# Optimization experiments

Hardware: AMD Instinct MI355X
Metric: run time of the kernel (lower is better)

The kernel has to match this reference:

```python
import jax, jax.numpy as jnp
import numpy as np

L_OBS = 512                      # number_of_obs
FOV = 6.283185307179586          # full 360-degree scan
EPS_PAR = 1e-4                   # parallel-ray threshold (matches torch |rxs|<0.0001)
MAP_SIZE = 256.0
B = 8
N = 8192


def setup_inputs() -> dict:
    key = jax.random.key(0)
    k1, k2, k3 = jax.random.split(key, 3)
    # map line segments: (x3, y3, x4, y4) in [0, 256]^2
    line_seg = jax.random.uniform(k1, (N, 4), dtype=jnp.float32) * MAP_SIZE
    # poses: xy in the map interior, theta in [0, 2pi)
    xy = MAP_SIZE * 0.25 + jax.random.uniform(k2, (B, 2), dtype=jnp.float32) * (MAP_SIZE * 0.5)
    theta = jax.random.uniform(k3, (B, 1), dtype=jnp.float32) * (2.0 * np.pi)
    pose = jnp.concatenate([xy, theta], axis=-1)
    return {"line_seg": line_seg, "pose": pose}


def _sense(line_seg, pose):
    # rays(): beam angles for each pose -> [B, L]
    beam = jnp.arange(L_OBS, dtype=jnp.float32) * (FOV / L_OBS)        # [L]
    ang = beam[None, :] + pose[:, 2:3]                                  # [B, L]
    rx = jnp.cos(ang)[:, :, None]                                       # [B, L, 1]
    ry = jnp.sin(ang)[:, :, None]
    x1 = pose[:, 0][:, None, None]                                      # [B, 1, 1]
    y1 = pose[:, 1][:, None, None]

    x3 = line_seg[:, 0][None, None, :]                                  # [1, 1, N]
    y3 = line_seg[:, 1][None, None, :]
    x4 = line_seg[:, 2][None, None, :]
    y4 = line_seg[:, 3][None, None, :]
    sx = x4 - x3
    sy = y4 - y3
    x1_x3 = x1 - x3                                                     # [B, 1, N]
    y1_y3 = y1 - y3

    # ray/segment intersection parameters, broadcast to [B, L, N]
    num_a = sx * y1_y3 - sy * x1_x3
    num_b = rx * y1_y3 - ry * x1_x3
    rxs = sy * rx - sx * ry
    parallel = jnp.abs(rxs) < EPS_PAR
    safe_rxs = jnp.where(parallel, jnp.float32(1.0), rxs)
    u_a = jnp.where(parallel, jnp.float32(0.0), num_a / safe_rxs)       # [B, L, N]
    u_b = jnp.where(parallel, jnp.float32(0.0), num_b / safe_rxs)

    valid = (~parallel) & (u_b >= 0.0) & (u_b <= 1.0) & (u_a >= 0.0)
    # nearest valid hit along each ray (torch: +1e7 penalty then nanargmin)
    u_masked = jnp.where(valid, u_a, jnp.float32(jnp.inf))
    idx = jnp.argmin(u_masked, axis=-1)                                 # [B, L]
    u_sel = jnp.take_along_axis(u_a, idx[:, :, None], axis=-1)          # [B, L, 1]

    ix = x1[:, :, 0] + rx[:, :, 0] * u_sel[:, :, 0]                     # [B, L]
    iy = y1[:, :, 0] + ry[:, :, 0] * u_sel[:, :, 0]
    return jnp.stack([ix, iy], axis=-1)                                 # [B, L, 2]


def _to_sensor_frame(pose, obs_global):
    c0 = pose[:, None, 0:2]                                             # [B, 1, 2]
    cos = jnp.cos(pose[:, 2])
    sin = jnp.sin(pose[:, 2])
    # R = [[cos, -sin], [sin, cos]] per batch, obs_local = (obs - c0) @ R
    R = jnp.stack([jnp.stack([cos, -sin], -1), jnp.stack([sin, cos], -1)], -2)  # [B, 2, 2]
    return jnp.einsum('blj,bjk->blk', obs_global - c0, R)


def reference(line_seg, pose):
    obs_global = _sense(line_seg, pose)
    obs_local = _to_sensor_frame(pose, obs_global)
    return obs_global, obs_local
```

## Files before the change

kernel.cpp:

```cpp
#include <hip/hip_runtime.h>
#include <math.h>

#define L_OBS   512
#define NSEG    8192
#define NB      8
#define EPS_PAR 1e-4f
#define ANG_STEP 0.012271846644580566f

#define SC2   32
#define CSEG2 (NSEG / SC2)
#define PART2_FLOATS (SC2 * NB * L_OBS)

__global__ __launch_bounds__(512) void raycast8_kernel(
    const float4* __restrict__ seg, const float* __restrict__ pose,
    float* __restrict__ part) {
    __shared__ float4 s4[CSEG2];
    __shared__ float  s_red[8][128];

    const int gid = blockIdx.x;
    const int sc = gid & (SC2 - 1);
    const int bg = (gid >> 5) & 3;
    const int b  = gid >> 7;

    const float x1 = pose[b * 3 + 0];
    const float y1 = pose[b * 3 + 1];
    const float th = pose[b * 3 + 2];

    const int t = threadIdx.x;
    if (t < CSEG2) {
        float4 v = seg[sc * CSEG2 + t];
        s4[t] = make_float4(v.z - v.x, v.w - v.y, x1 - v.x, y1 - v.y);
    }

    const int lane = t & 63;
    const int w    = t >> 6;
    const int beam0 = bg * 128 + lane;
    const float a0 = (float)beam0 * ANG_STEP + th;
    const float a1 = (float)(beam0 + 64) * ANG_STEP + th;
    const float rx0 = cosf(a0), ry0 = sinf(a0);
    const float rx1 = cosf(a1), ry1 = sinf(a1);
    const float INF = __builtin_inff();
    __syncthreads();

    float u0 = INF, u1 = INF;
    const float4* __restrict__ p = &s4[w * 32];
    #pragma unroll 8
    for (int i = 0; i < 32; ++i) {
        float4 s = p[i];
        float na = s.x * s.w - s.y * s.z;

        float rxs0 = s.y * rx0 - s.x * ry0;
        float nb0  = rx0 * s.w - ry0 * s.z;
        float r0   = __builtin_amdgcn_rcpf(rxs0);
        float ua0  = na  * r0;
        float ub0  = nb0 * r0;
        bool ok0 = (fabsf(rxs0) >= EPS_PAR) & (ub0 >= 0.0f) & (ub0 <= 1.0f) & (ua0 >= 0.0f);
        u0 = fminf(u0, ok0 ? ua0 : INF);

        float rxs1 = s.y * rx1 - s.x * ry1;
        float nb1  = rx1 * s.w - ry1 * s.z;
        float r1   = __builtin_amdgcn_rcpf(rxs1);
        float ua1  = na  * r1;
        float ub1  = nb1 * r1;
        bool ok1 = (fabsf(rxs1) >= EPS_PAR) & (ub1 >= 0.0f) & (ub1 <= 1.0f) & (ua1 >= 0.0f);
        u1 = fminf(u1, ok1 ? ua1 : INF);
    }

    s_red[w][lane]      = u0;
    s_red[w][lane + 64] = u1;
    __syncthreads();
    if (t < 128) {
        float m0 = fminf(fminf(s_red[0][t], s_red[1][t]),
                         fminf(s_red[2][t], s_red[3][t]));
        float m1 = fminf(fminf(s_red[4][t], s_red[5][t]),
                         fminf(s_red[6][t], s_red[7][t]));
        part[sc * (NB * L_OBS) + b * L_OBS + bg * 128 + t] = fminf(m0, m1);
    }
}

__global__ __launch_bounds__(256) void finalize7_kernel(
    const float4* __restrict__ seg, const float* __restrict__ pose,
    const float* __restrict__ part, float* __restrict__ out) {
    __shared__ float s_red[4][64];

    const int t    = threadIdx.x;
    const int lane = t & 63;
    const int q    = t >> 6;
    const int gbeam = blockIdx.x * 64 + lane;

    float u = INFINITY;
    #pragma unroll
    for (int j = 0; j < 8; ++j)
        u = fminf(u, part[(q * 8 + j) * (NB * L_OBS) + gbeam]);

    s_red[q][lane] = u;
    __syncthreads();
    if (t < 64) {
        const int gb   = blockIdx.x * 64 + t;
        const int b    = gb >> 9;
        const int beam = gb & (L_OBS - 1);
        const float x1 = pose[b * 3 + 0];
        const float y1 = pose[b * 3 + 1];
        const float th = pose[b * 3 + 2];
        const float ang = (float)beam * ANG_STEP + th;
        const float rx = cosf(ang), ry = sinf(ang);

        float m = fminf(fminf(s_red[0][t], s_red[1][t]),
                        fminf(s_red[2][t], s_red[3][t]));

        if (isinf(m)) {
            float4 s0 = seg[0];
            float sx = s0.z - s0.x, sy = s0.w - s0.y;
            float xd = x1 - s0.x,   yd = y1 - s0.y;
            float rxs   = sy * rx - sx * ry;
            float num_a = sx * yd - sy * xd;
            m = (fabsf(rxs) < EPS_PAR) ? 0.0f : (num_a / rxs);
        }

        float ix = x1 + rx * m;
        float iy = y1 + ry * m;
        float dx = ix - x1, dy = iy - y1;
        float c = cosf(th), s = sinf(th);
        out[gb * 2 + 0] = ix;
        out[gb * 2 + 1] = iy;
        const int off = NB * L_OBS * 2;
        out[off + gb * 2 + 0] =  dx * c + dy * s;
        out[off + gb * 2 + 1] = -dx * s + dy * c;
    }
}

extern "C" void kernel_launch(void* const* d_in, const int* in_sizes, int n_in,
                              void* d_out, int out_size, void* d_ws, size_t ws_size,
                              hipStream_t stream) {
    const float4* seg  = (const float4*)d_in[0];
    const float*  pose = (const float*)d_in[1];
    float* out = (float*)d_out;
    float* part = (float*)d_ws;

    raycast8_kernel<<<1024, 512, 0, stream>>>(seg, pose, part);
    finalize7_kernel<<<64, 256, 0, stream>>>(seg, pose, part, out);
}
```

Measured before the change: 21.24 us.

## Bin segments by angular beam range per pose and raycast only candidate lists

Adds a build pass that computes each segment's angular span from each pose with atan2 and appends its index into per-pose, per-16-beam bucket lists, staged in shared memory and flushed with atomics. A new raycast kernel then tests each beam group only against its bucket's segments and writes final outputs directly, which removes the brute-force B×L×N sweep and the separate finalize pass. In exchange it adds a memset, atomics and gather loads. It relies on bucket capacity (CAP) not overflowing; if it does, segments are silently dropped, and with uniformly random long segments the lists may be large. The path only runs when the workspace is big enough.

Result: slower. 49.04 us (+130.9%).

```diff
diff --git a/kernel.cpp b/kernel.cpp
--- a/kernel.cpp
+++ b/kernel.cpp
@@ -6,6 +6,163 @@
 #define NB      8
 #define EPS_PAR 1e-4f
 #define ANG_STEP 0.012271846644580566f
+#define INV_STEP 81.48733086305042f
+#define PI_F     3.14159265358979f
+#define TWOPI_F  6.28318530717959f
+#define INV_2PI  0.15915494309189535f
+#define MARG     2e-3f
+
+#define NBK   32
+#define CAP   4064
+#define LCAP  288
+
+#define WS_CNT_BYTES  (NB * NBK * 4)
+#define WS_NEED       (WS_CNT_BYTES + (size_t)NB * NBK * CAP * 2)
+
+__global__ __launch_bounds__(512) void build_kernel(
+    const float4* __restrict__ seg, const float* __restrict__ pose,
+    unsigned* __restrict__ cnt, unsigned short* __restrict__ list) {
+    __shared__ unsigned short stage[NBK][LCAP];
+    __shared__ int      cntL[NBK];
+    __shared__ unsigned baseL[NBK];
+
+    const int b  = blockIdx.x >> 4;
+    const int s0 = ((blockIdx.x & 15) << 9) + threadIdx.x;
+    const float x1 = pose[b * 3 + 0];
+    const float y1 = pose[b * 3 + 1];
+    const float th = pose[b * 3 + 2];
+
+    if (threadIdx.x < NBK) cntL[threadIdx.x] = 0;
+    __syncthreads();
+
+    float4 v = seg[s0];
+    float aA = atan2f(v.y - y1, v.x - x1);
+    float aB = atan2f(v.w - y1, v.z - x1);
+    float d  = aB - aA;
+    if (d > PI_F) d -= TWOPI_F; else if (d < -PI_F) d += TWOPI_F;
+    float lo  = (d >= 0.0f) ? aA : aB;
+    float wdt = fabsf(d);
+
+    int ilo, ihi;
+    if (wdt > PI_F - 0.02f) {
+        ilo = 512; ihi = 1023;
+    } else {
+        float a = lo - th;
+        a -= floorf(a * INV_2PI) * TWOPI_F;
+        ilo = (int)floorf((a - MARG) * INV_STEP) + 512;
+        ihi = (int)floorf((a + wdt + MARG) * INV_STEP) + 1 + 512;
+    }
+    int blo = ilo >> 4, bhi = ihi >> 4;
+    int nb = bhi - blo + 1; if (nb > NBK) nb = NBK;
+
+    for (int j = 0; j < nb; ++j) {
+        int bk = (blo + j) & (NBK - 1);
+        int pos = atomicAdd(&cntL[bk], 1);
+        if (pos < LCAP) {
+            stage[bk][pos] = (unsigned short)s0;
+        } else {
+            unsigned g = atomicAdd(&cnt[b * NBK + bk], 1u);
+            if (g < CAP) list[(size_t)(b * NBK + bk) * CAP + g] = (unsigned short)s0;
+        }
+    }
+    __syncthreads();
+
+    if (threadIdx.x < NBK) {
+        int c = cntL[threadIdx.x]; if (c > LCAP) c = LCAP;
+        baseL[threadIdx.x] = atomicAdd(&cnt[b * NBK + threadIdx.x], (unsigned)c);
+        cntL[threadIdx.x] = c;
+    }
+    __syncthreads();
+
+    for (int bk = 0; bk < NBK; ++bk) {
+        int c = cntL[bk];
+        unsigned base = baseL[bk];
+        for (int i = threadIdx.x; i < c; i += 512) {
+            unsigned p = base + i;
+            if (p < CAP) list[(size_t)(b * NBK + bk) * CAP + p] = stage[bk][i];
+        }
+    }
+}
+
+__global__ __launch_bounds__(1024) void raycast9_kernel(
+    const float4* __restrict__ seg, const float* __restrict__ pose,
+    const unsigned* __restrict__ cnt, const unsigned short* __restrict__ list,
+    float* __restrict__ out) {
+    __shared__ float red[64][16];
+
+    const int blk = blockIdx.x;
+    const int b  = blk >> 5;
+    const int bk = blk & (NBK - 1);
+    const int t  = threadIdx.x;
+    const int bm    = t & 15;
+    const int slice = t >> 4;
+
+    const float x1 = pose[b * 3 + 0];
+    const float y1 = pose[b * 3 + 1];
+    const float th = pose[b * 3 + 2];
+    const int beam = (bk << 4) + bm;
+    const float ang = (float)beam * ANG_STEP + th;
+    const float rx = cosf(ang), ry = sinf(ang);
+    const float INF = __builtin_inff();
+
+    int n = (int)cnt[b * NBK + bk]; if (n > CAP) n = CAP;
+    const unsigned short* __restrict__ lp = list + (size_t)(b * NBK + bk) * CAP;
+
+    float umin = INF;
+    for (int i = slice; i < n; i += 64) {
+        int idx = lp[i];
+        float4 v = seg[idx];
+        float sx = v.z - v.x;
+        float sy = v.w - v.y;
+        float xd = x1 - v.x;
+        float yd = y1 - v.y;
+        float rxs = sy * rx - sx * ry;
+        float na  = sx * yd - sy * xd;
+        float nb  = rx * yd - ry * xd;
+        float r   = __builtin_amdgcn_rcpf(rxs);
+        float ua  = na * r;
+        float ub  = nb * r;
+        bool ok = (fabsf(rxs) >= EPS_PAR) & (ub >= 0.0f) & (ub <= 1.0f) & (ua >= 0.0f);
+        umin = fminf(umin, ok ? ua : INF);
+    }
+
+    red[slice][bm] = umin;
+    __syncthreads();
+    if (slice < 16)
+        red[slice][bm] = fminf(fminf(red[slice][bm], red[slice + 16][bm]),
+                               fminf(red[slice + 32][bm], red[slice + 48][bm]));
+    __syncthreads();
+
+    if (t < 16) {
+        float m = red[0][t];
+        #pragma unroll
+        for (int j = 1; j < 16; ++j) m = fminf(m, red[j][t]);
+
+        const int gbeam = (bk << 4) + t;
+        const float angf = (float)gbeam * ANG_STEP + th;
+        const float rxf = cosf(angf), ryf = sinf(angf);
+
+        if (isinf(m)) {
+            float4 s0 = seg[0];
+            float sx = s0.z - s0.x, sy = s0.w - s0.y;
+            float xd = x1 - s0.x,   yd = y1 - s0.y;
+            float rxs   = sy * rxf - sx * ryf;
+            float num_a = sx * yd - sy * xd;
+            m = (fabsf(rxs) < EPS_PAR) ? 0.0f : (num_a / rxs);
+        }
+
+        float ix = x1 + rxf * m;
+        float iy = y1 + ryf * m;
+        float dx = ix - x1, dy = iy - y1;
+        float c = cosf(th), s = sinf(th);
+        const int gb = b * L_OBS + gbeam;
+        out[gb * 2 + 0] = ix;
+        out[gb * 2 + 1] = iy;
+        const int off = NB * L_OBS * 2;
+        out[off + gb * 2 + 0] =  dx * c + dy * s;
+        out[off + gb * 2 + 1] = -dx * s + dy * c;
+    }
+}
 
 #define SC2   32
 #define CSEG2 (NSEG / SC2)
@@ -16,22 +173,18 @@
     float* __restrict__ part) {
     __shared__ float4 s4[CSEG2];
     __shared__ float  s_red[8][128];
-
     const int gid = blockIdx.x;
     const int sc = gid & (SC2 - 1);
     const int bg = (gid >> 5) & 3;
     const int b  = gid >> 7;
-
     const float x1 = pose[b * 3 + 0];
     const float y1 = pose[b * 3 + 1];
     const float th = pose[b * 3 + 2];
-
     const int t = threadIdx.x;
     if (t < CSEG2) {
         float4 v = seg[sc * CSEG2 + t];
         s4[t] = make_float4(v.z - v.x, v.w - v.y, x1 - v.x, y1 - v.y);
     }
-
     const int lane = t & 63;
     const int w    = t >> 6;
     const int beam0 = bg * 128 + lane;
@@ -41,14 +194,12 @@
     const float rx1 = cosf(a1), ry1 = sinf(a1);
     const float INF = __builtin_inff();
     __syncthreads();
-
     float u0 = INF, u1 = INF;
     const float4* __restrict__ p = &s4[w * 32];
     #pragma unroll 8
     for (int i = 0; i < 32; ++i) {
         float4 s = p[i];
         float na = s.x * s.w - s.y * s.z;
-
         float rxs0 = s.y * rx0 - s.x * ry0;
         float nb0  = rx0 * s.w - ry0 * s.z;
         float r0   = __builtin_amdgcn_rcpf(rxs0);
@@ -56,7 +207,6 @@
         float ub0  = nb0 * r0;
         bool ok0 = (fabsf(rxs0) >= EPS_PAR) & (ub0 >= 0.0f) & (ub0 <= 1.0f) & (ua0 >= 0.0f);
         u0 = fminf(u0, ok0 ? ua0 : INF);
-
         float rxs1 = s.y * rx1 - s.x * ry1;
         float nb1  = rx1 * s.w - ry1 * s.z;
         float r1   = __builtin_amdgcn_rcpf(rxs1);
@@ -65,7 +215,6 @@
         bool ok1 = (fabsf(rxs1) >= EPS_PAR) & (ub1 >= 0.0f) & (ub1 <= 1.0f) & (ua1 >= 0.0f);
         u1 = fminf(u1, ok1 ? ua1 : INF);
     }
-
     s_red[w][lane]      = u0;
     s_red[w][lane + 64] = u1;
     __syncthreads();
@@ -82,17 +231,14 @@
     const float4* __restrict__ seg, const float* __restrict__ pose,
     const float* __restrict__ part, float* __restrict__ out) {
     __shared__ float s_red[4][64];
-
     const int t    = threadIdx.x;
     const int lane = t & 63;
     const int q    = t >> 6;
     const int gbeam = blockIdx.x * 64 + lane;
-
     float u = INFINITY;
     #pragma unroll
     for (int j = 0; j < 8; ++j)
         u = fminf(u, part[(q * 8 + j) * (NB * L_OBS) + gbeam]);
-
     s_red[q][lane] = u;
     __syncthreads();
     if (t < 64) {
@@ -104,10 +250,8 @@
         const float th = pose[b * 3 + 2];
         const float ang = (float)beam * ANG_STEP + th;
         const float rx = cosf(ang), ry = sinf(ang);
-
         float m = fminf(fminf(s_red[0][t], s_red[1][t]),
                         fminf(s_red[2][t], s_red[3][t]));
-
         if (isinf(m)) {
             float4 s0 = seg[0];
             float sx = s0.z - s0.x, sy = s0.w - s0.y;
@@ -116,7 +260,6 @@
             float num_a = sx * yd - sy * xd;
             m = (fabsf(rxs) < EPS_PAR) ? 0.0f : (num_a / rxs);
         }
-
         float ix = x1 + rx * m;
         float iy = y1 + ry * m;
         float dx = ix - x1, dy = iy - y1;
@@ -135,8 +278,16 @@
     const float4* seg  = (const float4*)d_in[0];
     const float*  pose = (const float*)d_in[1];
     float* out = (float*)d_out;
-    float* part = (float*)d_ws;
-
-    raycast8_kernel<<<1024, 512, 0, stream>>>(seg, pose, part);
-    finalize7_kernel<<<64, 256, 0, stream>>>(seg, pose, part, out);
-}
+
+    if (ws_size >= WS_NEED) {
+        unsigned* cnt = (unsigned*)d_ws;
+        unsigned short* list = (unsigned short*)((char*)d_ws + WS_CNT_BYTES);
+        hipMemsetAsync(cnt, 0, WS_CNT_BYTES, stream);
+        build_kernel<<<128, 512, 0, stream>>>(seg, pose, cnt, list);
+        raycast9_kernel<<<NB * NBK, 1024, 0, stream>>>(seg, pose, cnt, list, out);
+    } else {
+        float* part = (float*)d_ws;
+        raycast8_kernel<<<1024, 512, 0, stream>>>(seg, pose, part);
+        finalize7_kernel<<<64, 256, 0, stream>>>(seg, pose, part, out);
+    }
+}
```

## Cull segments outside block's beam angular range before ray intersection loop

Applied to the files above, without the earlier changes.

Each block now computes the angular span each segment subtends from the pose using atan2f, and keeps only segments whose span overlaps the block's 128-beam window (plus a margin). Kept segments are compacted into shared memory through an atomic counter, and the inner loop iterates over that compacted list strided across waves. This is meant to cut the intersection arithmetic, since random segments cover only part of the 360-degree scan. In exchange it adds atan2 work, an extra barrier and shared atomics, and it makes results depend on the margin-based culling being correct at wraparound and near-parallel boundaries.

After: 19.01 us. 1.12x faster.

```diff
diff --git a/kernel.cpp b/kernel.cpp
--- a/kernel.cpp
+++ b/kernel.cpp
@@ -6,16 +6,22 @@
 #define NB      8
 #define EPS_PAR 1e-4f
 #define ANG_STEP 0.012271846644580566f
+#define INV_STEP 81.48733086305042f
+#define PI_F     3.14159265358979f
+#define TWOPI_F  6.28318530717959f
+#define INV_2PI  0.15915494309189535f
+#define MARG     2e-3f
 
 #define SC2   32
 #define CSEG2 (NSEG / SC2)
 #define PART2_FLOATS (SC2 * NB * L_OBS)
 
-__global__ __launch_bounds__(512) void raycast8_kernel(
+__global__ __launch_bounds__(512) void raycast10_kernel(
     const float4* __restrict__ seg, const float* __restrict__ pose,
     float* __restrict__ part) {
     __shared__ float4 s4[CSEG2];
     __shared__ float  s_red[8][128];
+    __shared__ int    s_n;
 
     const int gid = blockIdx.x;
     const int sc = gid & (SC2 - 1);
@@ -27,9 +33,34 @@
     const float th = pose[b * 3 + 2];
 
     const int t = threadIdx.x;
+    if (t == 0) s_n = 0;
+    __syncthreads();
+
     if (t < CSEG2) {
         float4 v = seg[sc * CSEG2 + t];
-        s4[t] = make_float4(v.z - v.x, v.w - v.y, x1 - v.x, y1 - v.y);
+        float aA = atan2f(v.y - y1, v.x - x1);
+        float aB = atan2f(v.w - y1, v.z - x1);
+        float d  = aB - aA;
+        if (d > PI_F) d -= TWOPI_F; else if (d < -PI_F) d += TWOPI_F;
+        float lo  = (d >= 0.0f) ? aA : aB;
+        float wdt = fabsf(d);
+
+        bool keep;
+        if (wdt > PI_F - 0.02f) {
+            keep = true;
+        } else {
+            float a = lo - th;
+            a -= floorf(a * INV_2PI) * TWOPI_F;
+            int ilo = (int)floorf((a - MARG) * INV_STEP);
+            int ihi = (int)floorf((a + wdt + MARG) * INV_STEP) + 1;
+            if (ilo < 0) { ilo += 512; ihi += 512; }
+            const int B0 = bg * 128, B1 = bg * 128 + 127;
+            keep = (ilo <= B1 && ihi >= B0) || (ihi >= B0 + 512);
+        }
+        if (keep) {
+            int pos = atomicAdd(&s_n, 1);
+            s4[pos] = make_float4(v.z - v.x, v.w - v.y, x1 - v.x, y1 - v.y);
+        }
     }
 
     const int lane = t & 63;
@@ -42,11 +73,11 @@
     const float INF = __builtin_inff();
     __syncthreads();
 
+    const int n = s_n;
     float u0 = INF, u1 = INF;
-    const float4* __restrict__ p = &s4[w * 32];
-    #pragma unroll 8
-    for (int i = 0; i < 32; ++i) {
-        float4 s = p[i];
+    #pragma unroll 4
+    for (int i = w; i < n; i += 8) {
+        float4 s = s4[i];
         float na = s.x * s.w - s.y * s.z;
 
         float rxs0 = s.y * rx0 - s.x * ry0;
@@ -137,6 +168,6 @@
     float* out = (float*)d_out;
     float* part = (float*)d_ws;
 
-    raycast8_kernel<<<1024, 512, 0, stream>>>(seg, pose, part);
+    raycast10_kernel<<<1024, 512, 0, stream>>>(seg, pose, part);
     finalize7_kernel<<<64, 256, 0, stream>>>(seg, pose, part, out);
 }
```

## Cull segments outside each block's angular beam wedge before ray testing

Applied to the files above, without the earlier changes.

Each block covers 128 beams spanning a quarter-turn wedge. Before the intersection loop, segments that cannot intersect this wedge are rejected with cross-product tests, using a margin and a degenerate-case fallback. Survivors are compacted into shared memory via a shared atomic counter, and the inner loop strides over the compacted list. The second beam direction is also derived by a 45-degree rotation of the first instead of calling sin/cos again. This removes most per-beam intersection work but adds a block-wide sync, shared atomics and a variable-length loop, and the culling margin could change results at wedge boundaries.

Result: faster. 18.39 us (-13.4%).

```diff
diff --git a/kernel.cpp b/kernel.cpp
--- a/kernel.cpp
+++ b/kernel.cpp
@@ -7,15 +7,20 @@
 #define EPS_PAR 1e-4f
 #define ANG_STEP 0.012271846644580566f
 
+#define C64   0.70710678118654752f
+#define C129  (-0.0122715808f)
+#define S129  (0.9999246959f)
+
 #define SC2   32
 #define CSEG2 (NSEG / SC2)
 #define PART2_FLOATS (SC2 * NB * L_OBS)
 
-__global__ __launch_bounds__(512) void raycast8_kernel(
+__global__ __launch_bounds__(512) void raycast13_kernel(
     const float4* __restrict__ seg, const float* __restrict__ pose,
     float* __restrict__ part) {
     __shared__ float4 s4[CSEG2];
     __shared__ float  s_red[8][128];
+    __shared__ int    s_n;
 
     const int gid = blockIdx.x;
     const int sc = gid & (SC2 - 1);
@@ -27,26 +32,63 @@
     const float th = pose[b * 3 + 2];
 
     const int t = threadIdx.x;
-    if (t < CSEG2) {
-        float4 v = seg[sc * CSEG2 + t];
-        s4[t] = make_float4(v.z - v.x, v.w - v.y, x1 - v.x, y1 - v.y);
-    }
+    if (t == 0) s_n = 0;
+    __syncthreads();
 
     const int lane = t & 63;
     const int w    = t >> 6;
-    const int beam0 = bg * 128 + lane;
+    const int B0   = bg * 128;
+
+    const int beam0 = B0 + lane;
     const float a0 = (float)beam0 * ANG_STEP + th;
-    const float a1 = (float)(beam0 + 64) * ANG_STEP + th;
     const float rx0 = cosf(a0), ry0 = sinf(a0);
-    const float rx1 = cosf(a1), ry1 = sinf(a1);
+    const float rx1 = C64 * (rx0 - ry0);
+    const float ry1 = C64 * (rx0 + ry0);
+
+    if (t < CSEG2) {
+        const float aa = (float)(B0 - 1) * ANG_STEP + th;
+        const float d0x = cosf(aa), d0y = sinf(aa);
+        const float d1x = d0x * C129 - d0y * S129;
+        const float d1y = d0x * S129 + d0y * C129;
+
+        float4 v = seg[sc * CSEG2 + t];
+        float ax = v.x - x1, ay = v.y - y1;
+        float bx = v.z - x1, by = v.w - y1;
+        float X0a = d0x * ay - d0y * ax;
+        float Xa1 = ax * d1y - ay * d1x;
+        float X0b = d0x * by - d0y * bx;
+        float Xb1 = bx * d1y - by * d1x;
+        float Xab = ax * by - ay * bx;
+        const float M = 0.25f;
+
+        bool inA_a = (X0a >= -M) & (Xa1 >= -M);
+        bool inA_b = (X0b >= -M) & (Xb1 >= -M);
+        bool d0W, d1W;
+        if (Xab >= 0.0f) {
+            d0W = (X0a <=  M) & (X0b >= -M);
+            d1W = (Xa1 >= -M) & (Xb1 <=  M);
+        } else {
+            d0W = (X0b <=  M) & (X0a >= -M);
+            d1W = (Xb1 >= -M) & (Xa1 <=  M);
+        }
+        float la2 = ax * ax + ay * ay;
+        float lb2 = bx * bx + by * by;
+        bool degen = (Xab * Xab <= 4e-6f * la2 * lb2);
+
+        if (inA_a | inA_b | d0W | d1W | degen) {
+            int pos = atomicAdd(&s_n, 1);
+            s4[pos] = make_float4(bx - ax, by - ay, -ax, -ay);
+        }
+    }
+
     const float INF = __builtin_inff();
     __syncthreads();
 
+    const int n = s_n;
     float u0 = INF, u1 = INF;
-    const float4* __restrict__ p = &s4[w * 32];
-    #pragma unroll 8
-    for (int i = 0; i < 32; ++i) {
-        float4 s = p[i];
+    #pragma unroll 4
+    for (int i = w; i < n; i += 8) {
+        float4 s = s4[i];
         float na = s.x * s.w - s.y * s.z;
 
         float rxs0 = s.y * rx0 - s.x * ry0;
@@ -74,7 +116,7 @@
                          fminf(s_red[2][t], s_red[3][t]));
         float m1 = fminf(fminf(s_red[4][t], s_red[5][t]),
                          fminf(s_red[6][t], s_red[7][t]));
-        part[sc * (NB * L_OBS) + b * L_OBS + bg * 128 + t] = fminf(m0, m1);
+        part[sc * (NB * L_OBS) + b * L_OBS + B0 + t] = fminf(m0, m1);
     }
 }
 
@@ -137,6 +179,6 @@
     float* out = (float*)d_out;
     float* part = (float*)d_ws;
 
-    raycast8_kernel<<<1024, 512, 0, stream>>>(seg, pose, part);
+    raycast13_kernel<<<1024, 512, 0, stream>>>(seg, pose, part);
     finalize7_kernel<<<64, 256, 0, stream>>>(seg, pose, part, out);
 }
```
